# Kernel tuning notes

Measured on AMD Instinct MI355X. Metric: run time of the kernel, lower is better.

## Reference

```python
import jax, jax.numpy as jnp
import numpy as np

C, DEPTH, HEADS, WS = 180, 6, 6, 16
CR, SQ, OVR, MLP_RATIO = 3, 30, 0.5, 2.0
CC = C // CR                      # 60 compressed channels
CSE = CC // (SQ // CR)            # 6 SE squeeze channels
HID = int(C * MLP_RATIO)          # 360 mlp hidden
OWS = int(WS * (1 + OVR))         # 24 overlapping window
HD = C // HEADS                   # 30 head dim


def _rel_index(ws):
    coords = np.stack(np.meshgrid(np.arange(ws), np.arange(ws), indexing='ij')).reshape(2, -1)
    rel = (coords[:, :, None] - coords[:, None, :]).transpose(1, 2, 0)
    rel[..., 0] += ws - 1; rel[..., 1] += ws - 1; rel[..., 0] *= 2 * ws - 1
    return jnp.asarray(rel.sum(-1))

REL_IDX = _rel_index(WS)  # (WS^2, WS^2) int


def _shift_mask(H, W, ws, ss):
    m = np.zeros((H, W), np.float32); cnt = 0
    sl = (slice(0, -ws), slice(-ws, -ss), slice(-ss, None))
    for h in sl:
        for w in sl:
            m[h, w] = cnt; cnt += 1
    mw = m.reshape(H // ws, ws, W // ws, ws).transpose(0, 2, 1, 3).reshape(-1, ws * ws)
    am = mw[:, None, :] - mw[:, :, None]
    return jnp.asarray(np.where(am != 0, -100.0, 0.0).astype(np.float32))  # (nW, N, N)


def _ln(x, w, b):
    mu = x.mean(-1, keepdims=True)
    var = ((x - mu) ** 2).mean(-1, keepdims=True)
    return (x - mu) * jax.lax.rsqrt(var + 1e-5) * w + b


def _wpart(x, ws):
    B, H, W, c = x.shape
    return x.reshape(B, H // ws, ws, W // ws, ws, c).transpose(0, 1, 3, 2, 4, 5).reshape(-1, ws, ws, c)


def _wrev(w, ws, H, W):
    B = w.shape[0] // ((H // ws) * (W // ws))
    return w.reshape(B, H // ws, W // ws, ws, ws, -1).transpose(0, 1, 3, 2, 4, 5).reshape(B, H, W, -1)


def _conv(x, w, b, pad):
    y = jax.lax.conv_general_dilated(x, w, (1, 1), [(pad, pad), (pad, pad)], dimension_numbers=('NCHW', 'OIHW', 'NCHW'))
    return y + b[None, :, None, None]


def _window_msa(xw, qkv_w, qkv_b, relb, pw, pb, mask):
    Bw, N, c = xw.shape
    qkv = (xw @ qkv_w + qkv_b).reshape(Bw, N, 3, HEADS, HD).transpose(2, 0, 3, 1, 4)
    q, k, v = qkv[0], qkv[1], qkv[2]
    attn = jnp.einsum('bhqd,bhkd->bhqk', q, k) * (HD ** -0.5)
    attn = attn + relb[REL_IDX].transpose(2, 0, 1)[None]  # relative position bias (h,N,N)
    if mask is not None:
        nW = mask.shape[0]
        attn = (attn.reshape(Bw // nW, nW, HEADS, N, N) + mask[None, :, None]).reshape(Bw, HEADS, N, N)
    attn = jax.nn.softmax(attn, axis=-1)
    out = jnp.einsum('bhqk,bhkd->bhqd', attn, v).transpose(0, 2, 1, 3).reshape(Bw, N, c)
    return out @ pw + pb


def _hab(x, H, W, shift, n1w, n1b, qkvw, qkvb, relb, pw, pb, ccw, ccb, ca1w, ca1b, ca2w, ca2b, cew, ceb, n2w, n2b, m1w, m1b, m2w, m2b):
    B, N, c = x.shape
    xn = _ln(x, n1w, n1b).reshape(B, H, W, c)
    if shift > 0:
        xn = jnp.roll(xn, (-shift, -shift), (1, 2))
    mask = _shift_mask(H, W, WS, shift) if shift > 0 else None
    wins = _wpart(xn, WS).reshape(-1, WS * WS, c)
    a = _window_msa(wins, qkvw, qkvb, relb, pw, pb, mask).reshape(-1, WS, WS, c)
    xa = _wrev(a, WS, H, W)
    if shift > 0:
        xa = jnp.roll(xa, (shift, shift), (1, 2))
    x = x + xa.reshape(B, N, c)
    feat = x.transpose(0, 2, 1).reshape(B, c, H, W)
    comp = _conv(feat, ccw, ccb, 1)       # (B,CC,H,W)
    s = comp.mean((2, 3))                 # SE squeeze (B,CC)
    g = jax.nn.sigmoid(jax.nn.relu(s @ ca1w + ca1b) @ ca2w + ca2b)
    ca = _conv(comp * g[:, :, None, None], cew, ceb, 1)
    x = x + ca.reshape(B, c, N).transpose(0, 2, 1)
    h = _ln(x, n2w, n2b)
    return x + jax.nn.gelu(h @ m1w + m1b, approximate=False) @ m2w + m2b


def _ocab(x, H, W, nw, nb, qw, qb, kvw, kvb, pw, pb):
    B, N, c = x.shape
    xn = _ln(x, nw, nb)
    feat = xn.transpose(0, 2, 1).reshape(B, c, H, W)
    q = _wpart(feat.transpose(0, 2, 3, 1), WS).reshape(-1, WS * WS, c) @ qw + qb
    pad = (OWS - WS) // 2
    fp = jnp.pad(feat, ((0, 0), (0, 0), (pad, pad), (pad, pad)))
    nWh, nWw = H // WS, W // WS
    ih = (np.arange(nWh) * WS)[:, None] + np.arange(OWS)[None, :]
    iw = (np.arange(nWw) * WS)[:, None] + np.arange(OWS)[None, :]
    patches = fp[:, :, ih[:, None, :, None], iw[None, :, None, :]]   # (B,c,nWh,nWw,OWS,OWS) = unfold
    kvf = patches.transpose(0, 2, 3, 4, 5, 1).reshape(B * nWh * nWw, OWS * OWS, c)
    k, v = jnp.split(kvf @ kvw + kvb, 2, axis=-1)
    Bn = kvf.shape[0]
    qh = q.reshape(Bn, WS * WS, HEADS, HD).transpose(0, 2, 1, 3)
    kh = k.reshape(Bn, OWS * OWS, HEADS, HD).transpose(0, 2, 1, 3)
    vh = v.reshape(Bn, OWS * OWS, HEADS, HD).transpose(0, 2, 1, 3)
    attn = jax.nn.softmax(jnp.einsum('bhqd,bhkd->bhqk', qh, kh) * (HD ** -0.5), axis=-1)
    out = jnp.einsum('bhqk,bhkd->bhqd', attn, vh).transpose(0, 2, 1, 3).reshape(Bn, WS * WS, c)
    out = _wrev((out @ pw + pb).reshape(-1, WS, WS, c), WS, H, W)
    return x + out.reshape(B, N, c)


def setup_inputs() -> dict:
    ks = iter(jax.random.split(jax.random.key(0), 40))
    def nrm(shape):
        return jax.random.normal(next(ks), shape, jnp.float32) * 0.02
    D = DEPTH
    return dict(
        x=jax.random.normal(next(ks), (1, 192 * 192, C), jnp.float32),
        hab_n1_w=jnp.ones((D, C)), hab_n1_b=jnp.zeros((D, C)),
        hab_qkv_w=nrm((D, C, 3 * C)), hab_qkv_b=jnp.zeros((D, 3 * C)),
        hab_relb=nrm((D, (2 * WS - 1) ** 2, HEADS)),
        hab_proj_w=nrm((D, C, C)), hab_proj_b=jnp.zeros((D, C)),
        hab_cc_w=nrm((D, CC, C, 3, 3)), hab_cc_b=jnp.zeros((D, CC)),
        hab_ca1_w=nrm((D, CC, CSE)), hab_ca1_b=jnp.zeros((D, CSE)),
        hab_ca2_w=nrm((D, CSE, CC)), hab_ca2_b=jnp.zeros((D, CC)),
        hab_ce_w=nrm((D, C, CC, 3, 3)), hab_ce_b=jnp.zeros((D, C)),
        hab_n2_w=jnp.ones((D, C)), hab_n2_b=jnp.zeros((D, C)),
        hab_m1_w=nrm((D, C, HID)), hab_m1_b=jnp.zeros((D, HID)),
        hab_m2_w=nrm((D, HID, C)), hab_m2_b=jnp.zeros((D, C)),
        ocab_n_w=jnp.ones((C,)), ocab_n_b=jnp.zeros((C,)),
        ocab_q_w=nrm((C, C)), ocab_q_b=jnp.zeros((C,)),
        ocab_kv_w=nrm((C, 2 * C)), ocab_kv_b=jnp.zeros((2 * C,)),
        ocab_p_w=nrm((C, C)), ocab_p_b=jnp.zeros((C,)),
        conv_w=nrm((C, C, 3, 3)), conv_b=jnp.zeros((C,)),
        H=192, W=192,
    )


def reference(x, hab_n1_w, hab_n1_b, hab_qkv_w, hab_qkv_b, hab_relb, hab_proj_w, hab_proj_b, hab_cc_w, hab_cc_b, hab_ca1_w, hab_ca1_b, hab_ca2_w, hab_ca2_b, hab_ce_w, hab_ce_b, hab_n2_w, hab_n2_b, hab_m1_w, hab_m1_b, hab_m2_w, hab_m2_b, ocab_n_w, ocab_n_b, ocab_q_w, ocab_q_b, ocab_kv_w, ocab_kv_b, ocab_p_w, ocab_p_b, conv_w, conv_b, H, W):
    B, N, c = x.shape
    shortcut = x
    for i in range(DEPTH):
        shift = 0 if i % 2 == 0 else WS // 2
        x = _hab(x, H, W, shift, hab_n1_w[i], hab_n1_b[i], hab_qkv_w[i], hab_qkv_b[i], hab_relb[i], hab_proj_w[i], hab_proj_b[i], hab_cc_w[i], hab_cc_b[i], hab_ca1_w[i], hab_ca1_b[i], hab_ca2_w[i], hab_ca2_b[i], hab_ce_w[i], hab_ce_b[i], hab_n2_w[i], hab_n2_b[i], hab_m1_w[i], hab_m1_b[i], hab_m2_w[i], hab_m2_b[i])
    x = _ocab(x, H, W, ocab_n_w, ocab_n_b, ocab_q_w, ocab_q_b, ocab_kv_w, ocab_kv_b, ocab_p_w, ocab_p_b)
    feat = _conv(x.transpose(0, 2, 1).reshape(B, c, H, W), conv_w, conv_b, 1)
    return shortcut + feat.reshape(B, c, N).transpose(0, 2, 1)
```

## Files before the change

kernel.cpp:

```cpp
#include <hip/hip_runtime.h>
#include <math.h>


#define DEV __device__ __forceinline__

constexpr int HH   = 192;
constexpr int WW   = 192;
constexpr int NT   = HH * WW;
constexpr int C    = 180;
constexpr int HEADS= 6;
constexpr int HD   = 30;
constexpr int WS   = 16;
constexpr int NWW  = WW / WS;
constexpr int NWIN = 144;
constexpr int NTW  = 256;
constexpr int OWS  = 24;
constexpr int NKV  = OWS*OWS;
constexpr int CCH  = 60;
constexpr int CSE  = 6;
constexpr int HID  = 360;
constexpr int DEPTH= 6;

typedef _Float16 h8   __attribute__((ext_vector_type(8)));
typedef _Float16 h4   __attribute__((ext_vector_type(4)));
typedef float    f32x4 __attribute__((ext_vector_type(4)));

constexpr int PKG     = 2560;
constexpr int PKCHUNK = 9 * 64 * 40;

constexpr int QKV_PL = 9*6*PKG;
constexpr int PROJ_PL= 3*6*PKG;
constexpr int M1_PL  = 6*6*PKG;
constexpr int M2_PL  = 3*12*PKG;
constexpr int OQ_PL  = 3*6*PKG;
constexpr int OKV_PL = 6*6*PKG;
constexpr int OP_PL  = 3*6*PKG;
constexpr int CC_PL  = 1*6*PKCHUNK;
constexpr int CE_PL  = 3*2*PKCHUNK;
constexpr int FIN_PL = 3*6*PKCHUNK;

constexpr size_t PO_QKV = 0;
constexpr size_t PO_PROJ= PO_QKV + 6ull*QKV_PL;
constexpr size_t PO_M1  = PO_PROJ+ 6ull*PROJ_PL;
constexpr size_t PO_M2  = PO_M1  + 6ull*M1_PL;
constexpr size_t PO_OQ  = PO_M2  + 6ull*M2_PL;
constexpr size_t PO_OKV = PO_OQ  + OQ_PL;
constexpr size_t PO_OP  = PO_OKV + OKV_PL;
constexpr size_t PO_CC  = PO_OP  + OP_PL;
constexpr size_t PO_CE  = PO_CC  + 6ull*CC_PL;
constexpr size_t PO_FIN = PO_CE  + 6ull*CE_PL;
constexpr size_t PK_HALFS = PO_FIN + FIN_PL;

constexpr size_t OFF_X    = 0;
constexpr size_t OFF_A    = OFF_X    + (size_t)NT*C;
constexpr size_t OFF_B    = OFF_A    + (size_t)NT*C;
constexpr size_t OFF_COMP = OFF_B    + (size_t)NT*C;
constexpr size_t OFF_S    = OFF_COMP + (size_t)NT*CCH;
constexpr size_t OFF_G    = OFF_S    + 64;
constexpr size_t OFF_QKV  = OFF_G    + 64;
constexpr size_t OFF_PK   = OFF_QKV  + 16000000;
constexpr size_t OFF_PB   = OFF_PK   + PK_HALFS/2 + 8;

DEV int win_to_nat(int r, int shift) {
  int w   = r >> 8;
  int pos = r & 255;
  int wh = w / NWW, ww = w - wh*NWW;
  int rh = wh*WS + (pos >> 4);
  int rw = ww*WS + (pos & 15);
  int sh = rh + shift; if (sh >= HH) sh -= HH;
  int sw = rw + shift; if (sw >= WW) sw -= WW;
  return sh*WW + sw;
}

DEV int ocab_src_row(int gr) {
  int w = gr / NKV;
  int t = gr - w*NKV;
  int wh = w / NWW, ww = w - wh*NWW;
  int i = t / OWS, j = t - i*OWS;
  int gh = wh*WS - 4 + i;
  int gw = ww*WS - 4 + j;
  if ((unsigned)gh >= (unsigned)HH || (unsigned)gw >= (unsigned)WW) return -1;
  return (((gh >> 4)*NWW + (gw >> 4)) << 8) + ((gh & 15) << 4) + (gw & 15);
}

DEV float gelu_exact(float v) {
  return 0.5f * v * (1.0f + erff(v * 0.70710678118654752f));
}

DEV int col_remap(int np, int mode) {
  if (mode == 0) return np;
  int d = np & 31, hh = (np >> 5) % 6;
  if (d >= 30) return -1;
  if (mode == 1) { int third = np / 192; return third*180 + hh*30 + d; }
  if (mode == 2) { int half  = np / 192; return half *180 + hh*30 + d; }
  return hh*30 + d;
}

__global__ __launch_bounds__(256) void pack_gemmw(
    const float* __restrict__ W, _Float16* __restrict__ Wp,
    int K, int N, int nch, int mode, float scale,
    int perLayer, int nlayers, int sstride)
{
  int idx = blockIdx.x * 256 + threadIdx.x;
  if (idx >= perLayer * nlayers) return;
  int layer = idx / perLayer;
  int rem = idx - layer*perLayer;
  int unit = rem / PKG;
  int r2 = rem - unit*PKG;
  int n64 = r2 / 40, kk = r2 - n64*40;
  int cb = unit / nch, ch = unit - cb*nch;
  int gk = ch*32 + kk;
  int np = cb*64 + n64;
  float v = 0.f;
  if (kk < 32 && gk < K) {
    int sc = col_remap(np, mode);
    if (sc >= 0 && sc < N)
      v = W[(size_t)layer*sstride + (size_t)gk*N + sc] * scale;
  }
  Wp[idx] = (_Float16)v;
}

__global__ __launch_bounds__(256) void pack_bias(
    const float* __restrict__ b, float* __restrict__ bp,
    int N, int Np, int mode, float scale, int nlayers)
{
  int idx = blockIdx.x * 256 + threadIdx.x;
  if (idx >= Np * nlayers) return;
  int layer = idx / Np, np = idx - layer*Np;
  int sc = col_remap(np, mode);
  bp[idx] = (sc >= 0 && sc < N) ? b[layer*N + sc] * scale : 0.f;
}

__global__ __launch_bounds__(256) void pack_convw(
    const float* __restrict__ Wc, _Float16* __restrict__ Wp,
    int IC, int OC, int nch, int perLayer, int nlayers, int sstride)
{
  int idx = blockIdx.x * 256 + threadIdx.x;
  if (idx >= perLayer * nlayers) return;
  int layer = idx / perLayer;
  int rem = idx - layer*perLayer;
  int kk = rem % 40;
  int r  = rem / 40;
  int oc = r & 63; r >>= 6;
  int tap = r % 9; r /= 9;
  int ch = r % nch; int cb = r / nch;
  float v = 0.f;
  int goc = cb*64 + oc, gk = ch*32 + kk;
  if (kk < 32 && goc < OC && gk < IC)
    v = Wc[(size_t)layer*sstride + ((size_t)goc * IC + gk) * 9 + tap];
  Wp[idx] = (_Float16)v;
}

__global__ __launch_bounds__(256) void ln2_kernel(
    const float* __restrict__ X, const float* __restrict__ gw,
    const float* __restrict__ gb, _Float16* __restrict__ OUT,
    int mode, int shift)
{
  int wave = threadIdx.x >> 6, lane = threadIdx.x & 63;
  int r = blockIdx.x * 4 + wave;
  int s = (mode == 1) ? win_to_nat(r, shift) : r;
  const float* xr = X + (size_t)s * C;
  float v0 = xr[lane];
  float v1 = xr[lane + 64];
  float v2 = (lane < C - 128) ? xr[lane + 128] : 0.f;
  float sum = v0 + v1 + v2;
  float sq  = v0*v0 + v1*v1 + v2*v2;
  #pragma unroll
  for (int off = 32; off > 0; off >>= 1) {
    sum += __shfl_down(sum, off);
    sq  += __shfl_down(sq,  off);
  }
  sum = __shfl(sum, 0);
  sq  = __shfl(sq,  0);
  float mu  = sum * (1.f / C);
  float var = sq * (1.f / C) - mu * mu;
  float inv = rsqrtf(var + 1e-5f);
  _Float16* orow = OUT + (size_t)r * 192;
  orow[lane]      = (_Float16)((v0 - mu) * inv * gw[lane]      + gb[lane]);
  orow[lane + 64] = (_Float16)((v1 - mu) * inv * gw[lane + 64] + gb[lane + 64]);
  if (lane < C - 128)
    orow[lane + 128] = (_Float16)((v2 - mu) * inv * gw[lane + 128] + gb[lane + 128]);
  if (lane < 12) orow[180 + lane] = (_Float16)0.f;
}

__global__ __launch_bounds__(256) void gemm2(
    const _Float16* __restrict__ A, int lda,
    const _Float16* __restrict__ Wp, const float* __restrict__ bias,
    _Float16* __restrict__ O16, int ldo, int nstore,
    float* __restrict__ O32, const float* __restrict__ RES,
    int K, int nch, int amap, int emap, int epi, int shift)
{
  __shared__ _Float16 As[128][40];
  __shared__ _Float16 Bs[64][40];
  int tid  = threadIdx.x;
  int lane = tid & 63, wave = tid >> 6;
  int quad = lane >> 4, ln16 = lane & 15;
  int row0 = blockIdx.y * 128;
  int col0 = blockIdx.x * 64;

  f32x4 acc[2][4];
  #pragma unroll
  for (int mt = 0; mt < 2; ++mt)
    #pragma unroll
    for (int nb = 0; nb < 4; ++nb)
      #pragma unroll
      for (int r = 0; r < 4; ++r) acc[mt][nb][r] = 0.f;

  int ar0 = tid >> 1;
  (void)ar0;

  for (int c = 0; c < nch; ++c) {
    int k0 = c * 32;
    #pragma unroll
    for (int i = 0; i < 2; ++i) {
      int task = i*256 + tid;
      int ar = task >> 2, ak = (task & 3) * 8;
      int gr = row0 + ar;
      int sr = amap ? ocab_src_row(gr) : gr;
      h8 av;
      #pragma unroll
      for (int j = 0; j < 8; ++j) av[j] = (_Float16)0.f;
      if (sr >= 0) {
        const _Float16* ap = A + (size_t)sr*lda + k0 + ak;
        if (k0 + ak + 8 <= K) av = *(const h8*)ap;
        else {
          #pragma unroll
          for (int j = 0; j < 8; ++j)
            if (k0 + ak + j < K) av[j] = ap[j];
        }
      }
      *(h8*)&As[ar][ak] = av;
    }
    {
      const h8* src = (const h8*)(Wp + (size_t)(blockIdx.x*nch + c) * PKG);
      h8* dst = (h8*)&Bs[0][0];
      dst[tid] = src[tid];
      if (tid < 64) dst[256 + tid] = src[256 + tid];
    }
    __syncthreads();
    h8 af0 = *(const h8*)&As[wave*32 + ln16][quad*8];
    h8 af1 = *(const h8*)&As[wave*32 + 16 + ln16][quad*8];
    #pragma unroll
    for (int nb = 0; nb < 4; ++nb) {
      h8 bf = *(const h8*)&Bs[nb*16 + ln16][quad*8];
      acc[0][nb] = __builtin_amdgcn_mfma_f32_16x16x32_f16(af0, bf, acc[0][nb], 0, 0, 0);
      acc[1][nb] = __builtin_amdgcn_mfma_f32_16x16x32_f16(af1, bf, acc[1][nb], 0, 0, 0);
    }
    __syncthreads();
  }

  #pragma unroll
  for (int mt = 0; mt < 2; ++mt)
    #pragma unroll
    for (int r = 0; r < 4; ++r) {
      int m = row0 + wave*32 + mt*16 + quad*4 + r;
      int dst = emap ? win_to_nat(m, shift) : m;
      #pragma unroll
      for (int nb = 0; nb < 4; ++nb) {
        int n = col0 + nb*16 + ln16;
        if (n < nstore) {
          float v = acc[mt][nb][r] + bias[n];
          if (epi == 2) {
            v += RES[(size_t)dst*180 + n];
            O32[(size_t)dst*180 + n] = v;
          } else {
            if (epi == 1) v = gelu_exact(v);
            O16[(size_t)dst*ldo + n] = (_Float16)v;
          }
        }
      }
    }
}

__global__ __launch_bounds__(256) void conv9_mfma(
    const float* __restrict__ Xf, const _Float16* __restrict__ Xh, int ldah,
    const _Float16* __restrict__ Wp, const float* __restrict__ bias,
    const float* __restrict__ scale, const float* __restrict__ RES,
    float* __restrict__ O32, _Float16* __restrict__ O16,
    int IC, int OC, int nch)
{
  __shared__ _Float16 hs[3][66][40];
  __shared__ _Float16 wsm[PKCHUNK];
  int tid  = threadIdx.x;
  int lane = tid & 63, wave = tid >> 6;
  int quad = lane >> 4, ln16 = lane & 15;
  int p0 = blockIdx.y * 64;
  int h  = p0 / WW;
  int w0 = p0 - h * WW;
  int col0 = blockIdx.x * 64;

  f32x4 acc[4];
  #pragma unroll
  for (int nb = 0; nb < 4; ++nb)
    #pragma unroll
    for (int r = 0; r < 4; ++r) acc[nb][r] = 0.f;

  for (int c = 0; c < nch; ++c) {
    int k0 = c * 32;
    {
      const h8* src = (const h8*)(Wp + (size_t)(blockIdx.x * nch + c) * PKCHUNK);
      h8* dst = (h8*)wsm;
      #pragma unroll 3
      for (int idx = tid; idx < PKCHUNK/8; idx += 256) dst[idx] = src[idx];
    }
    for (int idx = tid; idx < 3*66*4; idx += 256) {
      int r    = idx / (66*4);
      int rem  = idx - r*(66*4);
      int px   = rem >> 2;
      int ks   = (rem & 3) * 8;
      int gh = h - 1 + r, gw = w0 - 1 + px;
      h8 hv;
      #pragma unroll
      for (int j = 0; j < 8; ++j) hv[j] = (_Float16)0.f;
      if ((unsigned)gh < (unsigned)HH && (unsigned)gw < (unsigned)WW) {
        if (Xh) {
          const _Float16* sp = Xh + (size_t)(gh*WW + gw) * ldah + k0 + ks;
          h8 t = *(const h8*)sp;
          if (scale) {
            #pragma unroll
            for (int j = 0; j < 8; ++j)
              hv[j] = (_Float16)((float)t[j] * scale[k0 + ks + j]);
          } else hv = t;
        } else {
          const float* sp = Xf + (size_t)(gh*WW + gw) * IC + k0 + ks;
          if (k0 + ks + 8 <= IC) {
            float4 q0 = *(const float4*)sp;
            float4 q1 = *(const float4*)(sp + 4);
            hv[0]=(_Float16)q0.x; hv[1]=(_Float16)q0.y; hv[2]=(_Float16)q0.z; hv[3]=(_Float16)q0.w;
            hv[4]=(_Float16)q1.x; hv[5]=(_Float16)q1.y; hv[6]=(_Float16)q1.z; hv[7]=(_Float16)q1.w;
          } else {
            #pragma unroll
            for (int j = 0; j < 8; ++j)
              if (k0 + ks + j < IC) hv[j] = (_Float16)sp[j];
          }
        }
      }
      *(h8*)&hs[r][px][ks] = hv;
    }
    __syncthreads();
    #pragma unroll
    for (int tap = 0; tap < 9; ++tap) {
      int dyy = tap / 3, dxt = tap % 3;
      h8 af = *(const h8*)&hs[dyy][wave*16 + ln16 + dxt][quad*8];
      #pragma unroll
      for (int nb = 0; nb < 4; ++nb) {
        h8 bf = *(const h8*)&wsm[(tap*64 + nb*16 + ln16)*40 + quad*8];
        acc[nb] = __builtin_amdgcn_mfma_f32_16x16x32_f16(af, bf, acc[nb], 0, 0, 0);
      }
    }
    __syncthreads();
  }

  #pragma unroll
  for (int r = 0; r < 4; ++r) {
    int p = p0 + wave*16 + quad*4 + r;
    #pragma unroll
    for (int nb = 0; nb < 4; ++nb) {
      int oc = col0 + nb*16 + ln16;
      if (O16) {
        float v = (oc < OC) ? acc[nb][r] + bias[oc] : 0.f;
        O16[(size_t)p*64 + oc] = (_Float16)v;
      } else if (oc < OC) {
        float v = acc[nb][r] + bias[oc] + RES[(size_t)p * OC + oc];
        O32[(size_t)p * OC + oc] = v;
      }
    }
  }
}

__global__ __launch_bounds__(256) void win_attn_mfma(
    const _Float16* __restrict__ QKV, const float* __restrict__ relb,
    _Float16* __restrict__ OUT, int shift)
{
  __shared__ _Float16 Kf[256][40];
  __shared__ _Float16 Vt[32][264];
  __shared__ _Float16 rbs[962];
  __shared__ unsigned char rg[256];
  int b = blockIdx.x;
  int w = b / HEADS, hd = b - (b / HEADS)*HEADS;
  int tid = threadIdx.x, lane = tid & 63, wave = tid >> 6;
  int quad = lane >> 4, ln16 = lane & 15;
  const _Float16* base = QKV + (size_t)(w*NTW)*576;

  #pragma unroll
  for (int i = 0; i < 4; ++i) {
    int task = i*256 + tid;
    int row = task >> 2, seg = (task & 3) * 8;
    *(h8*)&Kf[row][seg] = *(const h8*)(base + (size_t)row*576 + 192 + hd*32 + seg);
    h8 hv = *(const h8*)(base + (size_t)row*576 + 384 + hd*32 + seg);
    #pragma unroll
    for (int j = 0; j < 8; ++j) Vt[seg + j][row] = hv[j];
  }
  for (int i = tid; i < 961; i += 256) rbs[i] = (_Float16)relb[i*HEADS + hd];
  if (shift > 0) {
    int wh = w / NWW, ww = w - wh*NWW;
    int rh = wh*WS + (tid >> 4), rw = ww*WS + (tid & 15);
    int regh = (rh < HH - WS) ? 0 : (rh < HH - 8 ? 1 : 2);
    int regw = (rw < WW - WS) ? 0 : (rw < WW - 8 ? 1 : 2);
    rg[tid] = (unsigned char)(regh*3 + regw);
  }

  h8 bq[4];
  #pragma unroll
  for (int qi = 0; qi < 4; ++qi) {
    int q = wave*64 + qi*16 + ln16;
    bq[qi] = *(const h8*)(base + (size_t)q*576 + hd*32 + quad*8);
  }
  __syncthreads();

  float mrun[4], lrun[4];
  f32x4 accO[4][2];
  #pragma unroll
  for (int qi = 0; qi < 4; ++qi) {
    mrun[qi] = -1e30f; lrun[qi] = 0.f;
    #pragma unroll
    for (int r = 0; r < 4; ++r) { accO[qi][0][r] = 0.f; accO[qi][1][r] = 0.f; }
  }
  int rgq[4] = {0,0,0,0};
  if (shift > 0) {
    #pragma unroll
    for (int qi = 0; qi < 4; ++qi) rgq[qi] = rg[wave*64 + qi*16 + ln16];
  }
  const f32x4 zero4 = {0.f,0.f,0.f,0.f};

  for (int kb = 0; kb < 4; ++kb) {
    f32x4 st[4][4];
    #pragma unroll
    for (int kt = 0; kt < 4; ++kt) {
      h8 ak = *(const h8*)&Kf[kb*64 + kt*16 + ln16][quad*8];
      #pragma unroll
      for (int qi = 0; qi < 4; ++qi)
        st[kt][qi] = __builtin_amdgcn_mfma_f32_16x16x32_f16(ak, bq[qi], zero4, 0, 0, 0);
    }
    #pragma unroll
    for (int qi = 0; qi < 4; ++qi) {
      int q = wave*64 + qi*16 + ln16;
      int qrr = q >> 4, qcc = q & 15;
      float bmax = -1e30f;
      #pragma unroll
      for (int kt = 0; kt < 4; ++kt) {
        int bidx0 = (qrr - (kb*4 + kt) + 15)*31 + qcc + 15 - quad*4;
        #pragma unroll
        for (int r = 0; r < 4; ++r) {
          float s = st[kt][qi][r] + (float)rbs[bidx0 - r];
          if (shift > 0) {
            int key = kb*64 + kt*16 + quad*4 + r;
            if (rg[key] != rgq[qi]) s -= 100.f;
          }
          st[kt][qi][r] = s;
          bmax = fmaxf(bmax, s);
        }
      }
      bmax = fmaxf(bmax, __shfl_xor(bmax, 16));
      bmax = fmaxf(bmax, __shfl_xor(bmax, 32));
      float mnew  = fmaxf(mrun[qi], bmax);
      float alpha = __expf(mrun[qi] - mnew);
      mrun[qi] = mnew;
      float ps = 0.f;
      #pragma unroll
      for (int kt = 0; kt < 4; ++kt)
        #pragma unroll
        for (int r = 0; r < 4; ++r) {
          float p = __expf(st[kt][qi][r] - mnew);
          st[kt][qi][r] = p; ps += p;
        }
      ps += __shfl_xor(ps, 16);
      ps += __shfl_xor(ps, 32);
      lrun[qi] = lrun[qi]*alpha + ps;
      #pragma unroll
      for (int r = 0; r < 4; ++r) {
        float fr = __shfl(alpha, quad*4 + r);
        accO[qi][0][r] *= fr;
        accO[qi][1][r] *= fr;
      }
    }
    #pragma unroll
    for (int kt = 0; kt < 4; ++kt) {
      int kbase = kb*64 + kt*16 + quad*4;
      h4 bv0 = *(const h4*)&Vt[ln16][kbase];
      h4 bv1 = *(const h4*)&Vt[16 + ln16][kbase];
      #pragma unroll
      for (int qi = 0; qi < 4; ++qi) {
        h4 ap;
        #pragma unroll
        for (int j = 0; j < 4; ++j) ap[j] = (_Float16)st[kt][qi][j];
        accO[qi][0] = __builtin_amdgcn_mfma_f32_16x16x16f16(ap, bv0, accO[qi][0], 0, 0, 0);
        accO[qi][1] = __builtin_amdgcn_mfma_f32_16x16x16f16(ap, bv1, accO[qi][1], 0, 0, 0);
      }
    }
  }

  #pragma unroll
  for (int qi = 0; qi < 4; ++qi) {
    float linv = 1.f / lrun[qi];
    #pragma unroll
    for (int r = 0; r < 4; ++r) {
      float fr = __shfl(linv, quad*4 + r);
      int q = wave*64 + qi*16 + quad*4 + r;
      _Float16* o = OUT + (size_t)(w*NTW + q)*192 + hd*HD;
      o[ln16] = (_Float16)(accO[qi][0][r] * fr);
      if (ln16 < HD - 16) o[16 + ln16] = (_Float16)(accO[qi][1][r] * fr);
    }
  }
}

__global__ __launch_bounds__(256) void ocab_attn_mfma(
    const _Float16* __restrict__ Q, const _Float16* __restrict__ KV,
    _Float16* __restrict__ OUT)
{
  constexpr int CH = 192;
  __shared__ _Float16 Kf[CH][40];
  __shared__ _Float16 Vt[32][200];
  int b = blockIdx.x;
  int w = b / HEADS, hd = b - (b / HEADS)*HEADS;
  int tid = threadIdx.x, lane = tid & 63, wave = tid >> 6;
  int quad = lane >> 4, ln16 = lane & 15;

  h8 bq[4];
  #pragma unroll
  for (int qi = 0; qi < 4; ++qi) {
    int q = wave*64 + qi*16 + ln16;
    bq[qi] = *(const h8*)(Q + (size_t)(w*NTW + q)*192 + hd*32 + quad*8);
  }

  float mrun[4], lrun[4];
  f32x4 accO[4][2];
  #pragma unroll
  for (int qi = 0; qi < 4; ++qi) {
    mrun[qi] = -1e30f; lrun[qi] = 0.f;
    #pragma unroll
    for (int r = 0; r < 4; ++r) { accO[qi][0][r] = 0.f; accO[qi][1][r] = 0.f; }
  }
  const f32x4 zero4 = {0.f,0.f,0.f,0.f};

  for (int ch = 0; ch < 3; ++ch) {
    __syncthreads();
    #pragma unroll
    for (int i = 0; i < 3; ++i) {
      int task = i*256 + tid;
      int row = task >> 2, seg = (task & 3) * 8;
      const _Float16* kvr = KV + (size_t)(w*NKV + ch*CH + row)*384;
      *(h8*)&Kf[row][seg] = *(const h8*)(kvr + hd*32 + seg);
      h8 hv = *(const h8*)(kvr + 192 + hd*32 + seg);
      #pragma unroll
      for (int j = 0; j < 8; ++j) Vt[seg + j][row] = hv[j];
    }
    __syncthreads();

    for (int kb = 0; kb < 3; ++kb) {
      f32x4 st[4][4];
      #pragma unroll
      for (int kt = 0; kt < 4; ++kt) {
        h8 ak = *(const h8*)&Kf[kb*64 + kt*16 + ln16][quad*8];
        #pragma unroll
        for (int qi = 0; qi < 4; ++qi)
          st[kt][qi] = __builtin_amdgcn_mfma_f32_16x16x32_f16(ak, bq[qi], zero4, 0, 0, 0);
      }
      #pragma unroll
      for (int qi = 0; qi < 4; ++qi) {
        float bmax = -1e30f;
        #pragma unroll
        for (int kt = 0; kt < 4; ++kt)
          #pragma unroll
          for (int r = 0; r < 4; ++r) bmax = fmaxf(bmax, st[kt][qi][r]);
        bmax = fmaxf(bmax, __shfl_xor(bmax, 16));
        bmax = fmaxf(bmax, __shfl_xor(bmax, 32));
        float mnew  = fmaxf(mrun[qi], bmax);
        float alpha = __expf(mrun[qi] - mnew);
        mrun[qi] = mnew;
        float ps = 0.f;
        #pragma unroll
        for (int kt = 0; kt < 4; ++kt)
          #pragma unroll
          for (int r = 0; r < 4; ++r) {
            float p = __expf(st[kt][qi][r] - mnew);
            st[kt][qi][r] = p; ps += p;
          }
        ps += __shfl_xor(ps, 16);
        ps += __shfl_xor(ps, 32);
        lrun[qi] = lrun[qi]*alpha + ps;
        #pragma unroll
        for (int r = 0; r < 4; ++r) {
          float fr = __shfl(alpha, quad*4 + r);
          accO[qi][0][r] *= fr;
          accO[qi][1][r] *= fr;
        }
      }
      #pragma unroll
      for (int kt = 0; kt < 4; ++kt) {
        int kbase = kb*64 + kt*16 + quad*4;
        h4 bv0 = *(const h4*)&Vt[ln16][kbase];
        h4 bv1 = *(const h4*)&Vt[16 + ln16][kbase];
        #pragma unroll
        for (int qi = 0; qi < 4; ++qi) {
          h4 ap;
          #pragma unroll
          for (int j = 0; j < 4; ++j) ap[j] = (_Float16)st[kt][qi][j];
          accO[qi][0] = __builtin_amdgcn_mfma_f32_16x16x16f16(ap, bv0, accO[qi][0], 0, 0, 0);
          accO[qi][1] = __builtin_amdgcn_mfma_f32_16x16x16f16(ap, bv1, accO[qi][1], 0, 0, 0);
        }
      }
    }
  }

  #pragma unroll
  for (int qi = 0; qi < 4; ++qi) {
    float linv = 1.f / lrun[qi];
    #pragma unroll
    for (int r = 0; r < 4; ++r) {
      float fr = __shfl(linv, quad*4 + r);
      int q = wave*64 + qi*16 + quad*4 + r;
      _Float16* o = OUT + (size_t)(w*NTW + q)*192 + hd*HD;
      o[ln16] = (_Float16)(accO[qi][0][r] * fr);
      if (ln16 < HD - 16) o[16 + ln16] = (_Float16)(accO[qi][1][r] * fr);
    }
  }
}

__global__ __launch_bounds__(256) void colsum_kernel(
    const _Float16* __restrict__ COMP, float* __restrict__ S)
{
  int tid = threadIdx.x;
  int seg = tid & 7, rb = tid >> 3;
  int row0 = blockIdx.x * 128;
  float a[8] = {};
  #pragma unroll
  for (int i = 0; i < 4; ++i) {
    int row = row0 + i*32 + rb;
    h8 v = *(const h8*)(COMP + (size_t)row*64 + seg*8);
    #pragma unroll
    for (int j = 0; j < 8; ++j) a[j] += (float)v[j];
  }
  __shared__ float sA[64];
  if (tid < 64) sA[tid] = 0.f;
  __syncthreads();
  #pragma unroll
  for (int j = 0; j < 8; ++j) atomicAdd(&sA[seg*8 + j], a[j]);
  __syncthreads();
  if (tid < 60) atomicAdd(&S[tid], sA[tid]);
}

__global__ __launch_bounds__(64) void se_kernel(
    const float* __restrict__ S, const float* __restrict__ w1,
    const float* __restrict__ b1, const float* __restrict__ w2,
    const float* __restrict__ b2, float* __restrict__ G)
{
  __shared__ float hid[CSE];
  int t = threadIdx.x;
  if (t < CSE) {
    float a = b1[t];
    for (int c = 0; c < CCH; ++c) a += (S[c] * (1.f/NT)) * w1[c * CSE + t];
    hid[t] = fmaxf(a, 0.f);
  }
  __syncthreads();
  if (t < CCH) {
    float a = b2[t];
    #pragma unroll
    for (int j = 0; j < CSE; ++j) a += hid[j] * w2[j * CCH + t];
    G[t] = 1.f / (1.f + __expf(-a));
  }
}


extern "C" void kernel_launch(void* const* d_in, const int* in_sizes, int n_in,
                              void* d_out, int out_size, void* d_ws, size_t ws_size,
                              hipStream_t stream) {
  const float* x_in   = (const float*)d_in[0];
  const float* n1w    = (const float*)d_in[1];
  const float* n1b    = (const float*)d_in[2];
  const float* qkvw   = (const float*)d_in[3];
  const float* qkvb   = (const float*)d_in[4];
  const float* relb   = (const float*)d_in[5];
  const float* projw  = (const float*)d_in[6];
  const float* projb  = (const float*)d_in[7];
  const float* ccw    = (const float*)d_in[8];
  const float* ccb    = (const float*)d_in[9];
  const float* ca1w   = (const float*)d_in[10];
  const float* ca1b   = (const float*)d_in[11];
  const float* ca2w   = (const float*)d_in[12];
  const float* ca2b   = (const float*)d_in[13];
  const float* cew    = (const float*)d_in[14];
  const float* ceb    = (const float*)d_in[15];
  const float* n2w    = (const float*)d_in[16];
  const float* n2b    = (const float*)d_in[17];
  const float* m1w    = (const float*)d_in[18];
  const float* m1b    = (const float*)d_in[19];
  const float* m2w    = (const float*)d_in[20];
  const float* m2b    = (const float*)d_in[21];
  const float* onw    = (const float*)d_in[22];
  const float* onb    = (const float*)d_in[23];
  const float* oqw    = (const float*)d_in[24];
  const float* oqb    = (const float*)d_in[25];
  const float* okvw   = (const float*)d_in[26];
  const float* okvb   = (const float*)d_in[27];
  const float* opw    = (const float*)d_in[28];
  const float* opb    = (const float*)d_in[29];
  const float* convw  = (const float*)d_in[30];
  const float* convb  = (const float*)d_in[31];

  float* ws   = (float*)d_ws;
  float*     X    = ws + OFF_X;
  _Float16*  A    = (_Float16*)(ws + OFF_A);
  _Float16*  Bq   = (_Float16*)(ws + OFF_B);
  _Float16*  COMP = (_Float16*)(ws + OFF_COMP);
  float*     S    = ws + OFF_S;
  float*     G    = ws + OFF_G;
  _Float16*  QKV  = (_Float16*)(ws + OFF_QKV);
  _Float16*  PK   = (_Float16*)(ws + OFF_PK);
  float*     PB   = ws + OFF_PB;

  float* qkvB = PB;
  float* oqB  = PB + 6*576;
  float* okvB = oqB + 192;

  const float scl = 0.18257418583505536f;

  (void)hipMemcpyAsync(X, x_in, (size_t)NT * C * sizeof(float),
                       hipMemcpyDeviceToDevice, stream);

  #define GRID(n) dim3(((n)+255)/256)
  pack_gemmw<<<GRID(6*QKV_PL), 256, 0, stream>>>(qkvw, PK+PO_QKV, 180, 540, 6, 1, 1.f, QKV_PL, 6, 180*540);
  pack_gemmw<<<GRID(6*PROJ_PL),256, 0, stream>>>(projw, PK+PO_PROJ,180, 180, 6, 0, 1.f, PROJ_PL,6, 180*180);
  pack_gemmw<<<GRID(6*M1_PL), 256, 0, stream>>>(m1w,  PK+PO_M1,  180, 360, 6, 0, 1.f, M1_PL,  6, 180*360);
  pack_gemmw<<<GRID(6*M2_PL), 256, 0, stream>>>(m2w,  PK+PO_M2,  360, 180,12, 0, 1.f, M2_PL,  6, 360*180);
  pack_gemmw<<<GRID(OQ_PL),   256, 0, stream>>>(oqw,  PK+PO_OQ,  180, 180, 6, 3, scl, OQ_PL,  1, 0);
  pack_gemmw<<<GRID(OKV_PL),  256, 0, stream>>>(okvw, PK+PO_OKV, 180, 360, 6, 2, 1.f, OKV_PL, 1, 0);
  pack_gemmw<<<GRID(OP_PL),   256, 0, stream>>>(opw,  PK+PO_OP,  180, 180, 6, 0, 1.f, OP_PL,  1, 0);
  pack_convw<<<GRID(6*CC_PL), 256, 0, stream>>>(ccw,  PK+PO_CC,  180,  60, 6, CC_PL, 6, 60*180*9);
  pack_convw<<<GRID(6*CE_PL), 256, 0, stream>>>(cew,  PK+PO_CE,   60, 180, 2, CE_PL, 6, 180*60*9);
  pack_convw<<<GRID(FIN_PL),  256, 0, stream>>>(convw,PK+PO_FIN, 180, 180, 6, FIN_PL,1, 0);
  pack_bias<<<GRID(6*576), 256, 0, stream>>>(qkvb, qkvB, 540, 576, 1, 1.f, 6);
  pack_bias<<<GRID(192),   256, 0, stream>>>(oqb,  oqB,  180, 192, 3, scl, 1);
  pack_bias<<<GRID(384),   256, 0, stream>>>(okvb, okvB, 360, 384, 2, 1.f, 1);

  const int MB128 = NT / 128;
  const int MB64  = NT / 64;

  for (int i = 0; i < DEPTH; ++i) {
    int shift = (i % 2 == 0) ? 0 : WS / 2;
    ln2_kernel<<<NT/4, 256, 0, stream>>>(X, n1w + i*C, n1b + i*C, A, 1, shift);
    gemm2<<<dim3(9, MB128), 256, 0, stream>>>(
        A, 192, PK+PO_QKV + (size_t)i*QKV_PL, qkvB + i*576,
        QKV, 576, 576, nullptr, nullptr, 180, 6, 0, 0, 0, 0);
    win_attn_mfma<<<NWIN*HEADS, 256, 0, stream>>>(
        QKV, relb + (size_t)i*961*HEADS, A, shift);
    gemm2<<<dim3(3, MB128), 256, 0, stream>>>(
        A, 192, PK+PO_PROJ + (size_t)i*PROJ_PL, projb + i*C,
        nullptr, 0, 180, X, X, 180, 6, 0, 1, 2, shift);
    conv9_mfma<<<dim3(1, MB64), 256, 0, stream>>>(
        X, nullptr, 0, PK+PO_CC + (size_t)i*CC_PL, ccb + i*CCH,
        nullptr, nullptr, nullptr, COMP, 180, 60, 6);
    (void)hipMemsetAsync(S, 0, 64*sizeof(float), stream);
    colsum_kernel<<<288, 256, 0, stream>>>(COMP, S);
    se_kernel<<<1, 64, 0, stream>>>(
        S, ca1w + (size_t)i*CCH*CSE, ca1b + (size_t)i*CSE,
        ca2w + (size_t)i*CSE*CCH, ca2b + (size_t)i*CCH, G);
    conv9_mfma<<<dim3(3, MB64), 256, 0, stream>>>(
        nullptr, COMP, 64, PK+PO_CE + (size_t)i*CE_PL, ceb + i*C,
        G, X, X, nullptr, 60, 180, 2);
    ln2_kernel<<<NT/4, 256, 0, stream>>>(X, n2w + i*C, n2b + i*C, A, 0, 0);
    gemm2<<<dim3(6, MB128), 256, 0, stream>>>(
        A, 192, PK+PO_M1 + (size_t)i*M1_PL, m1b + i*HID,
        QKV, 384, 360, nullptr, nullptr, 180, 6, 0, 0, 1, 0);
    gemm2<<<dim3(3, MB128), 256, 0, stream>>>(
        QKV, 384, PK+PO_M2 + (size_t)i*M2_PL, m2b + i*C,
        nullptr, 0, 180, X, X, 360, 12, 0, 0, 2, 0);
  }

  ln2_kernel<<<NT/4, 256, 0, stream>>>(X, onw, onb, A, 1, 0);
  gemm2<<<dim3(3, MB128), 256, 0, stream>>>(
      A, 192, PK+PO_OQ, oqB, Bq, 192, 192, nullptr, nullptr, 180, 6, 0, 0, 0, 0);
  gemm2<<<dim3(6, NWIN*NKV/128), 256, 0, stream>>>(
      A, 192, PK+PO_OKV, okvB, QKV, 384, 384, nullptr, nullptr, 180, 6, 1, 0, 0, 0);
  ocab_attn_mfma<<<NWIN*HEADS, 256, 0, stream>>>(Bq, QKV, A);
  gemm2<<<dim3(3, MB128), 256, 0, stream>>>(
      A, 192, PK+PO_OP, opb, nullptr, 0, 180, X, X, 180, 6, 0, 1, 2, 0);

  conv9_mfma<<<dim3(3, MB64), 256, 0, stream>>>(
      X, nullptr, 0, PK+PO_FIN, convb, nullptr, x_in,
      (float*)d_out, nullptr, 180, 180, 6);
}
```

Before: 2.829 ms.

## Pack weights in MFMA lane order and load B fragments directly to registers

Weight packing is reorganized so each lane's 8-half B fragment is contiguous in global memory, which drops the padded 40-wide LDS layout. The GEMM and 3x3 conv kernels now read B fragments straight from global/L2 into registers instead of staging them through shared memory. The conv kernel also prefetches the next tap's fragments, and the trailing barrier is moved to the start of the next iteration. This cuts LDS traffic, LDS footprint and one barrier per chunk, which could raise occupancy. The cost is that every wave re-reads the same weights from cache, and load latency is only partly hidden.

```diff
diff --git a/kernel.cpp b/kernel.cpp
--- a/kernel.cpp
+++ b/kernel.cpp
@@ -25,8 +25,8 @@
 typedef _Float16 h4   __attribute__((ext_vector_type(4)));
 typedef float    f32x4 __attribute__((ext_vector_type(4)));
 
-constexpr int PKG     = 2560;
-constexpr int PKCHUNK = 9 * 64 * 40;
+constexpr int PKG = 2048;
+constexpr int PKC = 18432;
 
 constexpr int QKV_PL = 9*6*PKG;
 constexpr int PROJ_PL= 3*6*PKG;
@@ -35,9 +35,9 @@
 constexpr int OQ_PL  = 3*6*PKG;
 constexpr int OKV_PL = 6*6*PKG;
 constexpr int OP_PL  = 3*6*PKG;
-constexpr int CC_PL  = 1*6*PKCHUNK;
-constexpr int CE_PL  = 3*2*PKCHUNK;
-constexpr int FIN_PL = 3*6*PKCHUNK;
+constexpr int CC_PL  = 1*6*PKC;
+constexpr int CE_PL  = 3*2*PKC;
+constexpr int FIN_PL = 3*6*PKC;
 
 constexpr size_t PO_QKV = 0;
 constexpr size_t PO_PROJ= PO_QKV + 6ull*QKV_PL;
@@ -105,14 +105,17 @@
   if (idx >= perLayer * nlayers) return;
   int layer = idx / perLayer;
   int rem = idx - layer*perLayer;
-  int unit = rem / PKG;
-  int r2 = rem - unit*PKG;
-  int n64 = r2 / 40, kk = r2 - n64*40;
+  int unit = rem >> 11;
+  int r2 = rem & 2047;
+  int nb = r2 >> 9;
+  int lane = (r2 >> 3) & 63;
+  int j = r2 & 7;
   int cb = unit / nch, ch = unit - cb*nch;
-  int gk = ch*32 + kk;
-  int np = cb*64 + n64;
+  int quad = lane >> 4, l16 = lane & 15;
+  int np = cb*64 + nb*16 + l16;
+  int gk = ch*32 + quad*8 + j;
   float v = 0.f;
-  if (kk < 32 && gk < K) {
+  if (gk < K) {
     int sc = col_remap(np, mode);
     if (sc >= 0 && sc < N)
       v = W[(size_t)layer*sstride + (size_t)gk*N + sc] * scale;
@@ -139,15 +142,20 @@
   if (idx >= perLayer * nlayers) return;
   int layer = idx / perLayer;
   int rem = idx - layer*perLayer;
-  int kk = rem % 40;
-  int r  = rem / 40;
-  int oc = r & 63; r >>= 6;
-  int tap = r % 9; r /= 9;
-  int ch = r % nch; int cb = r / nch;
+  int unit = rem / PKC;
+  int w2 = rem - unit*PKC;
+  int tap = w2 >> 11;
+  int r2 = w2 & 2047;
+  int nb = r2 >> 9;
+  int lane = (r2 >> 3) & 63;
+  int j = r2 & 7;
+  int cb = unit / nch, ch = unit - cb*nch;
+  int quad = lane >> 4, l16 = lane & 15;
+  int oc = cb*64 + nb*16 + l16;
+  int gk = ch*32 + quad*8 + j;
   float v = 0.f;
-  int goc = cb*64 + oc, gk = ch*32 + kk;
-  if (kk < 32 && goc < OC && gk < IC)
-    v = Wc[(size_t)layer*sstride + ((size_t)goc * IC + gk) * 9 + tap];
+  if (oc < OC && gk < IC)
+    v = Wc[(size_t)layer*sstride + ((size_t)oc * IC + gk) * 9 + tap];
   Wp[idx] = (_Float16)v;
 }
 
@@ -191,7 +199,6 @@
     int K, int nch, int amap, int emap, int epi, int shift)
 {
   __shared__ _Float16 As[128][40];
-  __shared__ _Float16 Bs[64][40];
   int tid  = threadIdx.x;
   int lane = tid & 63, wave = tid >> 6;
   int quad = lane >> 4, ln16 = lane & 15;
@@ -206,11 +213,11 @@
       #pragma unroll
       for (int r = 0; r < 4; ++r) acc[mt][nb][r] = 0.f;
 
-  int ar0 = tid >> 1;
-  (void)ar0;
+  const _Float16* wlane = Wp + (size_t)lane*8;
 
   for (int c = 0; c < nch; ++c) {
     int k0 = c * 32;
+    if (c) __syncthreads();
     #pragma unroll
     for (int i = 0; i < 2; ++i) {
       int task = i*256 + tid;
@@ -231,22 +238,18 @@
       }
       *(h8*)&As[ar][ak] = av;
     }
-    {
-      const h8* src = (const h8*)(Wp + (size_t)(blockIdx.x*nch + c) * PKG);
-      h8* dst = (h8*)&Bs[0][0];
-      dst[tid] = src[tid];
-      if (tid < 64) dst[256 + tid] = src[256 + tid];
-    }
+    h8 bf[4];
+    #pragma unroll
+    for (int nb = 0; nb < 4; ++nb)
+      bf[nb] = *(const h8*)(wlane + (size_t)(blockIdx.x*nch + c)*PKG + (size_t)nb*512);
     __syncthreads();
     h8 af0 = *(const h8*)&As[wave*32 + ln16][quad*8];
     h8 af1 = *(const h8*)&As[wave*32 + 16 + ln16][quad*8];
     #pragma unroll
     for (int nb = 0; nb < 4; ++nb) {
-      h8 bf = *(const h8*)&Bs[nb*16 + ln16][quad*8];
-      acc[0][nb] = __builtin_amdgcn_mfma_f32_16x16x32_f16(af0, bf, acc[0][nb], 0, 0, 0);
-      acc[1][nb] = __builtin_amdgcn_mfma_f32_16x16x32_f16(af1, bf, acc[1][nb], 0, 0, 0);
-    }
-    __syncthreads();
+      acc[0][nb] = __builtin_amdgcn_mfma_f32_16x16x32_f16(af0, bf[nb], acc[0][nb], 0, 0, 0);
+      acc[1][nb] = __builtin_amdgcn_mfma_f32_16x16x32_f16(af1, bf[nb], acc[1][nb], 0, 0, 0);
+    }
   }
 
   #pragma unroll
@@ -280,7 +283,6 @@
     int IC, int OC, int nch)
 {
   __shared__ _Float16 hs[3][66][40];
-  __shared__ _Float16 wsm[PKCHUNK];
   int tid  = threadIdx.x;
   int lane = tid & 63, wave = tid >> 6;
   int quad = lane >> 4, ln16 = lane & 15;
@@ -297,12 +299,7 @@
 
   for (int c = 0; c < nch; ++c) {
     int k0 = c * 32;
-    {
-      const h8* src = (const h8*)(Wp + (size_t)(blockIdx.x * nch + c) * PKCHUNK);
-      h8* dst = (h8*)wsm;
-      #pragma unroll 3
-      for (int idx = tid; idx < PKCHUNK/8; idx += 256) dst[idx] = src[idx];
-    }
+    if (c) __syncthreads();
     for (int idx = tid; idx < 3*66*4; idx += 256) {
       int r    = idx / (66*4);
       int rem  = idx - r*(66*4);
@@ -338,17 +335,30 @@
       *(h8*)&hs[r][px][ks] = hv;
     }
     __syncthreads();
+
+    const _Float16* wpc = Wp + (size_t)(blockIdx.x*nch + c) * PKC + (size_t)lane*8;
+    h8 bf[4];
+    #pragma unroll
+    for (int nb = 0; nb < 4; ++nb)
+      bf[nb] = *(const h8*)(wpc + (size_t)nb*512);
     #pragma unroll
     for (int tap = 0; tap < 9; ++tap) {
-      int dyy = tap / 3, dxt = tap % 3;
+      h8 bfn[4];
+      if (tap < 8) {
+        #pragma unroll
+        for (int nb = 0; nb < 4; ++nb)
+          bfn[nb] = *(const h8*)(wpc + (size_t)(tap+1)*2048 + (size_t)nb*512);
+      }
+      int dyy = tap / 3, dxt = tap - dyy*3;
       h8 af = *(const h8*)&hs[dyy][wave*16 + ln16 + dxt][quad*8];
       #pragma unroll
-      for (int nb = 0; nb < 4; ++nb) {
-        h8 bf = *(const h8*)&wsm[(tap*64 + nb*16 + ln16)*40 + quad*8];
-        acc[nb] = __builtin_amdgcn_mfma_f32_16x16x32_f16(af, bf, acc[nb], 0, 0, 0);
-      }
-    }
-    __syncthreads();
+      for (int nb = 0; nb < 4; ++nb)
+        acc[nb] = __builtin_amdgcn_mfma_f32_16x16x32_f16(af, bf[nb], acc[nb], 0, 0, 0);
+      if (tap < 8) {
+        #pragma unroll
+        for (int nb = 0; nb < 4; ++nb) bf[nb] = bfn[nb];
+      }
+    }
   }
 
   #pragma unroll
```

After: 2.483 ms. 12.2% less time.
